# Kernel tuning notes

Measured on AMD Instinct MI355X. Metric: run time of the kernel, lower is better.

The kernel has to match this reference:

```python
import jax, jax.numpy as jnp
import numpy as np

N = 4_000_000

def setup_inputs() -> dict:
    key = jax.random.key(0)
    k1, k2 = jax.random.split(key)
    quaternions = jax.random.normal(k1, (N, 4), dtype=jnp.float32)
    scales = jax.random.uniform(k2, (N, 3), dtype=jnp.float32)
    return {"quaternions": quaternions, "scales": scales}

def _build_rotation(q):
    # q: [N,4] already normalized, (r, x, y, z) convention as in 3DGS build_rotation
    r, x, y, z = q[:, 0], q[:, 1], q[:, 2], q[:, 3]
    R = jnp.stack([
        1 - 2 * (y * y + z * z), 2 * (x * y - r * z),     2 * (x * z + r * y),
        2 * (x * y + r * z),     1 - 2 * (x * x + z * z), 2 * (y * z - r * x),
        2 * (x * z - r * y),     2 * (y * z + r * x),     1 - 2 * (x * x + y * y),
    ], axis=-1)  # [N,9]
    return R.reshape(-1, 3, 3)

def reference(quaternions, scales):
    # F.normalize(p=2, dim=1) with eps clamp
    norm = jnp.maximum(jnp.linalg.norm(quaternions, axis=1, keepdims=True), 1e-12)
    q = quaternions / norm
    R = _build_rotation(q)                      # [N,3,3]
    M = R * scales[:, None, :]                  # R @ diag(scales), [N,3,3]
    covariance = jnp.einsum('nij,nkj->nik', M, M)  # M @ M^T
    return covariance
```

## Files before the change

kernel.cpp:

```cpp
#include <hip/hip_runtime.h>
#include <hip/hip_bf16.h>


__global__ __launch_bounds__(256) void gaussians_cov_kernel(
    const float4* __restrict__ quat,
    const float*  __restrict__ scales,
    float*        __restrict__ out,
    int n)
{
    int i = blockIdx.x * blockDim.x + threadIdx.x;
    if (i >= n) return;

    float4 q = quat[i];
    float r = q.x, x = q.y, y = q.z, z = q.w;

    float nrm = sqrtf(r*r + x*x + y*y + z*z);
    nrm = fmaxf(nrm, 1e-12f);
    float inv = 1.0f / nrm;
    r *= inv; x *= inv; y *= inv; z *= inv;

    const float* sp = scales + 3ll * i;
    float sx = sp[0], sy = sp[1], sz = sp[2];

    float R00 = 1.0f - 2.0f*(y*y + z*z);
    float R01 = 2.0f*(x*y - r*z);
    float R02 = 2.0f*(x*z + r*y);
    float R10 = 2.0f*(x*y + r*z);
    float R11 = 1.0f - 2.0f*(x*x + z*z);
    float R12 = 2.0f*(y*z - r*x);
    float R20 = 2.0f*(x*z - r*y);
    float R21 = 2.0f*(y*z + r*x);
    float R22 = 1.0f - 2.0f*(x*x + y*y);

    float sx2 = sx*sx, sy2 = sy*sy, sz2 = sz*sz;

    float c00 = R00*R00*sx2 + R01*R01*sy2 + R02*R02*sz2;
    float c01 = R00*R10*sx2 + R01*R11*sy2 + R02*R12*sz2;
    float c02 = R00*R20*sx2 + R01*R21*sy2 + R02*R22*sz2;
    float c11 = R10*R10*sx2 + R11*R11*sy2 + R12*R12*sz2;
    float c12 = R10*R20*sx2 + R11*R21*sy2 + R12*R22*sz2;
    float c22 = R20*R20*sx2 + R21*R21*sy2 + R22*R22*sz2;

    float* op = out + 9ll * i;
    op[0] = c00; op[1] = c01; op[2] = c02;
    op[3] = c01; op[4] = c11; op[5] = c12;
    op[6] = c02; op[7] = c12; op[8] = c22;
}

extern "C" void kernel_launch(void* const* d_in, const int* in_sizes, int n_in,
                              void* d_out, int out_size, void* d_ws, size_t ws_size,
                              hipStream_t stream)
{
    const float4* quat   = (const float4*)d_in[0];
    const float*  scales = (const float*)d_in[1];
    float*        out    = (float*)d_out;
    int n = in_sizes[0] / 4;

    int block = 256;
    int grid  = (n + block - 1) / block;
    gaussians_cov_kernel<<<grid, block, 0, stream>>>(quat, scales, out, n);
}
```

Before: 232.4 us.

## Stage scales and covariance output through LDS for coalesced vector accesses

Full blocks load their scales as contiguous float4 into shared memory and write the 9-float covariance results into shared memory. Each block then streams the results out as coalesced float4 stores. This replaces the strided 3-float loads and 9-float stores per thread, which the change targets as the main memory cost. It adds two barriers and about 12KB of LDS per block, and keeps a scalar fallback for the tail block.

```diff
diff --git a/kernel.cpp b/kernel.cpp
--- a/kernel.cpp
+++ b/kernel.cpp
@@ -2,25 +2,16 @@
 #include <hip/hip_bf16.h>
 
 
-__global__ __launch_bounds__(256) void gaussians_cov_kernel(
-    const float4* __restrict__ quat,
-    const float*  __restrict__ scales,
-    float*        __restrict__ out,
-    int n)
+#define BLK 256
+
+__device__ __forceinline__ void compute_cov(float4 q, float sx, float sy, float sz,
+                                            float* c )
 {
-    int i = blockIdx.x * blockDim.x + threadIdx.x;
-    if (i >= n) return;
-
-    float4 q = quat[i];
     float r = q.x, x = q.y, y = q.z, z = q.w;
-
     float nrm = sqrtf(r*r + x*x + y*y + z*z);
     nrm = fmaxf(nrm, 1e-12f);
     float inv = 1.0f / nrm;
     r *= inv; x *= inv; y *= inv; z *= inv;
-
-    const float* sp = scales + 3ll * i;
-    float sx = sp[0], sy = sp[1], sz = sp[2];
 
     float R00 = 1.0f - 2.0f*(y*y + z*z);
     float R01 = 2.0f*(x*y - r*z);
@@ -34,17 +25,65 @@
 
     float sx2 = sx*sx, sy2 = sy*sy, sz2 = sz*sz;
 
-    float c00 = R00*R00*sx2 + R01*R01*sy2 + R02*R02*sz2;
-    float c01 = R00*R10*sx2 + R01*R11*sy2 + R02*R12*sz2;
-    float c02 = R00*R20*sx2 + R01*R21*sy2 + R02*R22*sz2;
-    float c11 = R10*R10*sx2 + R11*R11*sy2 + R12*R12*sz2;
-    float c12 = R10*R20*sx2 + R11*R21*sy2 + R12*R22*sz2;
-    float c22 = R20*R20*sx2 + R21*R21*sy2 + R22*R22*sz2;
+    c[0] = R00*R00*sx2 + R01*R01*sy2 + R02*R02*sz2;
+    c[1] = R00*R10*sx2 + R01*R11*sy2 + R02*R12*sz2;
+    c[2] = R00*R20*sx2 + R01*R21*sy2 + R02*R22*sz2;
+    c[3] = R10*R10*sx2 + R11*R11*sy2 + R12*R12*sz2;
+    c[4] = R10*R20*sx2 + R11*R21*sy2 + R12*R22*sz2;
+    c[5] = R20*R20*sx2 + R21*R21*sy2 + R22*R22*sz2;
+}
 
-    float* op = out + 9ll * i;
-    op[0] = c00; op[1] = c01; op[2] = c02;
-    op[3] = c01; op[4] = c11; op[5] = c12;
-    op[6] = c02; op[7] = c12; op[8] = c22;
+__global__ __launch_bounds__(BLK) void gaussians_cov_kernel(
+    const float4* __restrict__ quat,
+    const float*  __restrict__ scales,
+    float*        __restrict__ out,
+    int n)
+{
+    __shared__ float s_sc[BLK * 3];
+    __shared__ float s_cov[BLK * 9];
+
+    const int t = threadIdx.x;
+    const long long base = (long long)blockIdx.x * BLK;
+
+    if (base + BLK <= n) {
+        if (t < (BLK * 3) / 4) {
+            ((float4*)s_sc)[t] =
+                ((const float4*)scales)[(long long)blockIdx.x * ((BLK * 3) / 4) + t];
+        }
+        float4 q = quat[base + t];
+        __syncthreads();
+
+        float sx = s_sc[3*t], sy = s_sc[3*t+1], sz = s_sc[3*t+2];
+
+        float c[6];
+        compute_cov(q, sx, sy, sz, c);
+
+        float* cp = s_cov + 9 * t;
+        cp[0] = c[0]; cp[1] = c[1]; cp[2] = c[2];
+        cp[3] = c[1]; cp[4] = c[3]; cp[5] = c[4];
+        cp[6] = c[2]; cp[7] = c[4]; cp[8] = c[5];
+        __syncthreads();
+
+        const float4* src = (const float4*)s_cov;
+        float4* dst = (float4*)(out + base * 9);
+        #pragma unroll
+        for (int k = 0; k < (BLK * 9) / 4; k += BLK) {
+            int idx = k + t;
+            if (idx < (BLK * 9) / 4) dst[idx] = src[idx];
+        }
+    } else {
+        long long i = base + t;
+        if (i < n) {
+            float4 q = quat[i];
+            const float* sp = scales + 3 * i;
+            float c[6];
+            compute_cov(q, sp[0], sp[1], sp[2], c);
+            float* op = out + 9 * i;
+            op[0] = c[0]; op[1] = c[1]; op[2] = c[2];
+            op[3] = c[1]; op[4] = c[3]; op[5] = c[4];
+            op[6] = c[2]; op[7] = c[4]; op[8] = c[5];
+        }
+    }
 }
 
 extern "C" void kernel_launch(void* const* d_in, const int* in_sizes, int n_in,
@@ -56,7 +95,6 @@
     float*        out    = (float*)d_out;
     int n = in_sizes[0] / 4;
 
-    int block = 256;
-    int grid  = (n + block - 1) / block;
-    gaussians_cov_kernel<<<grid, block, 0, stream>>>(quat, scales, out, n);
+    int grid = (n + BLK - 1) / BLK;
+    gaussians_cov_kernel<<<grid, BLK, 0, stream>>>(quat, scales, out, n);
 }
```

Result: faster. 225.4 us (-3.0%).
